# Kernel optimization log

Hardware: AMD Instinct MI355X
Metric: run time of the kernel (lower is better)

The kernel has to match this reference:

```python
import jax, jax.numpy as jnp
import numpy as np

B, S, H, DH = 8, 2048, 16, 64
D = H * DH  # 1024; also the input feature dim
BIG_NEG = 1e8


def setup_inputs() -> dict:
    key = jax.random.key(0)
    ks = jax.random.split(key, 7)
    glorot = lambda k, shp: jax.random.normal(k, shp, jnp.float32) * np.sqrt(2.0 / (shp[0] + shp[1]))
    return {
        "Q_seq": jax.random.normal(ks[0], (B, S, D), jnp.float32),
        "K_seq": jax.random.normal(ks[1], (B, S, D), jnp.float32),
        "Q_mask": jnp.ones((B, S), jnp.float32),
        "K_mask": jnp.ones((B, S), jnp.float32),
        "WQ": glorot(ks[2], (D, D)),
        "WK": glorot(ks[3], (D, D)),
        "Wq": glorot(ks[4], (D, H)),
        "Wk": glorot(ks[5], (D, H)),
        "WP": glorot(ks[6], (D, D)),
    }


def reference(Q_seq, B_K_seq=None, **_unused):
    raise NotImplementedError  # placeholder overwritten below


def reference(Q_seq, K_seq, Q_mask, K_mask, WQ, WK, Wq, Wk, WP):
    scale = 1.0 / (DH ** 0.5)
    b, s, _ = Q_seq.shape

    Q = Q_seq @ WQ                                        # (B,S,D)
    # query additive attention over the sequence, per head
    q_logits = jnp.einsum('bsd,dh->bhs', Q, Wq) * scale   # (B,H,S)
    q_logits = q_logits - (1.0 - Q_mask[:, None, :]) * BIG_NEG
    q_att = jax.nn.softmax(q_logits, axis=-1)

    Qh = Q.reshape(b, s, H, DH).transpose(0, 2, 1, 3)     # (B,H,S,DH)
    Kh = (K_seq @ WK).reshape(b, s, H, DH).transpose(0, 2, 1, 3)

    global_q = jnp.einsum('bhs,bhsd->bhd', q_att, Qh)     # (B,H,DH)
    QK = Kh * global_q[:, :, None, :]                     # (B,H,S,DH)

    # NOTE: original reshapes (B,H,S,DH) straight to (B,S,H*DH) WITHOUT a
    # transpose (head-mixing raw reshape) — replicated faithfully here.
    QK_flat = QK.reshape(b, s, H * DH)
    k_logits = jnp.einsum('bsd,dh->bhs', QK_flat, Wk) * scale
    k_logits = k_logits - (1.0 - K_mask[:, None, :]) * BIG_NEG
    k_att = jax.nn.softmax(k_logits, axis=-1)

    global_k = jnp.einsum('bhs,bhsd->bhd', k_att, QK)     # (B,H,DH)
    QKQ = global_k[:, :, None, :] * Qh                    # (B,H,S,DH)

    out = QKQ.transpose(0, 2, 1, 3).reshape(b, s, H * DH) @ WP
    out = out.reshape(b, s, H, DH).transpose(0, 2, 1, 3) + Qh   # (B,H,S,DH)
    out = out.transpose(0, 2, 1, 3).reshape(b, s, H * DH)       # (B,S,D)
    return out
```

## Files before the change

kernel.cpp:

```cpp
#include <hip/hip_runtime.h>
#include <cstdint>
#include <cstddef>


#define B_ 8
#define S_ 2048
#define H_ 16
#define D_ 1024
#define SCALE_ 0.125f
#define BIGNEG_ 1e8f

typedef __attribute__((ext_vector_type(8))) __bf16 bf16x8;
typedef __attribute__((ext_vector_type(4))) float f32x4;

__device__ __forceinline__ unsigned short f2bf(float f) {
  unsigned int u = __float_as_uint(f);
  u += 0x7FFFu + ((u >> 16) & 1u);
  return (unsigned short)(u >> 16);
}
__device__ __forceinline__ float bf2f(unsigned short h) {
  return __uint_as_float(((unsigned int)h) << 16);
}

__device__ __forceinline__ void gll16(const void* g, void* l) {
  __builtin_amdgcn_global_load_lds(
      (__attribute__((address_space(1))) void*)(uintptr_t)g,
      (__attribute__((address_space(3))) void*)(uintptr_t)l,
      16, 0, 0);
}

__global__ __launch_bounds__(256) void k_conv2(
    const float* __restrict__ in0, unsigned short* __restrict__ out0,
    const float* __restrict__ in1, unsigned short* __restrict__ out1, int n4) {
  int i = blockIdx.x * 256 + threadIdx.x;
  const float* in = in0;
  unsigned short* out = out0;
  if (i >= n4) { i -= n4; in = in1; out = out1; }
  float4 v = ((const float4*)in)[i];
  ushort4 o;
  o.x = f2bf(v.x); o.y = f2bf(v.y); o.z = f2bf(v.z); o.w = f2bf(v.w);
  ((ushort4*)out)[i] = o;
}

__global__ __launch_bounds__(256) void k_transpose3(
    const float* __restrict__ s0, unsigned short* __restrict__ d0,
    const float* __restrict__ s1, unsigned short* __restrict__ d1,
    const float* __restrict__ s2, unsigned short* __restrict__ d2,
    int K, int N) {
  const float* src = blockIdx.z == 0 ? s0 : (blockIdx.z == 1 ? s1 : s2);
  unsigned short* dst = blockIdx.z == 0 ? d0 : (blockIdx.z == 1 ? d1 : d2);
  __shared__ float tile[32][33];
  int n0 = blockIdx.x * 32, k0 = blockIdx.y * 32;
  int tx = threadIdx.x, ty = threadIdx.y;
#pragma unroll
  for (int i = 0; i < 4; i++) {
    int r = ty + i * 8;
    if (k0 + r < K && n0 + tx < N) tile[r][tx] = src[(size_t)(k0 + r) * N + n0 + tx];
  }
  __syncthreads();
#pragma unroll
  for (int i = 0; i < 4; i++) {
    int rn = ty + i * 8;
    if (n0 + rn < N && k0 + tx < K)
      dst[(size_t)(n0 + rn) * K + k0 + tx] = f2bf(tile[tx][rn]);
  }
}

__global__ __launch_bounds__(256) void k_transpose2(
    const float* __restrict__ s0, unsigned short* __restrict__ d0,
    const float* __restrict__ s1, unsigned short* __restrict__ d1,
    int K, int N) {
  const float* src = blockIdx.z == 0 ? s0 : s1;
  unsigned short* dst = blockIdx.z == 0 ? d0 : d1;
  __shared__ float tile[32][33];
  int n0 = blockIdx.x * 32, k0 = blockIdx.y * 32;
  int tx = threadIdx.x, ty = threadIdx.y;
#pragma unroll
  for (int i = 0; i < 4; i++) {
    int r = ty + i * 8;
    if (k0 + r < K && n0 + tx < N) tile[r][tx] = src[(size_t)(k0 + r) * N + n0 + tx];
  }
  __syncthreads();
#pragma unroll
  for (int i = 0; i < 4; i++) {
    int rn = ty + i * 8;
    if (n0 + rn < N && k0 + tx < K)
      dst[(size_t)(n0 + rn) * K + k0 + tx] = f2bf(tile[tx][rn]);
  }
}

__global__ __launch_bounds__(512, 2) void k_gemm256(
    const unsigned short* __restrict__ A, const unsigned short* __restrict__ Aalt,
    int asplit,
    const unsigned short* __restrict__ BTa, const unsigned short* __restrict__ BTb,
    int bstride, int bshift,
    unsigned short* __restrict__ Cbf, unsigned short* __restrict__ Calt,
    float* __restrict__ Cf, const unsigned short* __restrict__ Res,
    int N, int K, int ntiles) {
  __shared__ unsigned short lds[32768];
  int t = threadIdx.x;
  int lid = (blockIdx.x & 7) * ((int)gridDim.x >> 3) + (blockIdx.x >> 3);
  int mt = lid / ntiles, nt = lid - mt * ntiles;
  const unsigned short* BT = BTa;
  unsigned short* Cb = Cbf;
  if (mt >= asplit) { mt -= asplit; A = Aalt; BT = BTb; Cb = Calt; }
  if (bstride) BT += (size_t)(mt >> bshift) * (size_t)bstride;
  int m0 = mt * 256, n0 = nt * 256;
  int lane = t & 63, w = t >> 6;
  int wr = (w >> 2) * 128;
  int wc = (w & 3) * 64;
  int mq = lane & 15, q = lane >> 4;

  f32x4 zero = {0.f, 0.f, 0.f, 0.f};
  f32x4 acc[8][4];
#pragma unroll
  for (int i = 0; i < 8; i++)
#pragma unroll
    for (int j = 0; j < 4; j++) acc[i][j] = zero;

  const unsigned short* gA[2];
  const unsigned short* gB[2];
  int oA[2], oB[2];
#pragma unroll
  for (int p = 0; p < 2; p++) {
    int g = t + p * 512;
    int row2 = g >> 3, pre = (g & 7) ^ (row2 & 7);
    int r = row2 * 2 + (pre >> 2), oct = pre & 3;
    gA[p] = A + (size_t)(m0 + r) * K + oct * 8;
    gB[p] = BT + (size_t)(n0 + r) * K + oct * 8;
    oA[p] = g * 8;
    oB[p] = 8192 + g * 8;
  }

  int sA8 = ((((mq & 1) << 2) | q) ^ (mq >> 1)) * 8;
  int ra = (wr >> 1) + (mq >> 1);
  int rb = (wc >> 1) + (mq >> 1);

  int NT = K >> 5;
#pragma unroll
  for (int p = 0; p < 2; p++) gll16(gA[p], &lds[oA[p]]);
#pragma unroll
  for (int p = 0; p < 2; p++) gll16(gB[p], &lds[oB[p]]);
#pragma unroll
  for (int p = 0; p < 2; p++) gll16(gA[p] + 32, &lds[16384 + oA[p]]);
#pragma unroll
  for (int p = 0; p < 2; p++) gll16(gB[p] + 32, &lds[16384 + oB[p]]);

  for (int it = 0; it < NT; ++it) {
    int lbase = (it & 1) << 14;
    if (it < NT - 1) {
      asm volatile("s_waitcnt vmcnt(4)" ::: "memory");
    } else {
      asm volatile("s_waitcnt vmcnt(0)" ::: "memory");
    }
    __builtin_amdgcn_s_barrier();
    __builtin_amdgcn_sched_barrier(0);

    const unsigned short* la = &lds[lbase];
    const unsigned short* lb = &lds[lbase + 8192];
    bf16x8 av[8], bv[4];
#pragma unroll
    for (int i = 0; i < 4; i++)
      av[i] = *(const bf16x8*)&la[(ra + i * 8) * 64 + sA8];
#pragma unroll
    for (int j = 0; j < 4; j++)
      bv[j] = *(const bf16x8*)&lb[(rb + j * 8) * 64 + sA8];
    __builtin_amdgcn_sched_barrier(0);
#pragma unroll
    for (int i = 4; i < 8; i++)
      av[i] = *(const bf16x8*)&la[(ra + i * 8) * 64 + sA8];
    __builtin_amdgcn_sched_barrier(0);

    asm volatile("s_waitcnt lgkmcnt(4)" ::: "memory");
    __builtin_amdgcn_sched_barrier(0);
    __builtin_amdgcn_s_setprio(1);
#pragma unroll
    for (int i = 0; i < 4; i++)
#pragma unroll
      for (int j = 0; j < 4; j++)
        acc[i][j] = __builtin_amdgcn_mfma_f32_16x16x32_bf16(av[i], bv[j], acc[i][j], 0, 0, 0);
    __builtin_amdgcn_s_setprio(0);
    __builtin_amdgcn_sched_barrier(0);

    asm volatile("s_waitcnt lgkmcnt(0)" ::: "memory");
    __builtin_amdgcn_sched_barrier(0);
    __builtin_amdgcn_s_barrier();
    __builtin_amdgcn_sched_barrier(0);

    if (it + 2 < NT) {
      int k0 = (it + 2) * 32;
#pragma unroll
      for (int p = 0; p < 2; p++) gll16(gA[p] + k0, &lds[lbase + oA[p]]);
#pragma unroll
      for (int p = 0; p < 2; p++) gll16(gB[p] + k0, &lds[lbase + oB[p]]);
    }

    __builtin_amdgcn_s_setprio(1);
#pragma unroll
    for (int i = 4; i < 8; i++)
#pragma unroll
      for (int j = 0; j < 4; j++)
        acc[i][j] = __builtin_amdgcn_mfma_f32_16x16x32_bf16(av[i], bv[j], acc[i][j], 0, 0, 0);
    __builtin_amdgcn_s_setprio(0);
  }

#pragma unroll
  for (int i = 0; i < 8; i++)
#pragma unroll
    for (int j = 0; j < 4; j++)
#pragma unroll
      for (int r = 0; r < 4; r++) {
        int row = m0 + wr + i * 16 + q * 4 + r;
        int col = n0 + wc + j * 16 + mq;
        size_t o = (size_t)row * N + col;
        float v = acc[i][j][r];
        if (Res) v += bf2f(Res[o]);
        if (Cf) Cf[o] = v;
        if (Cb) Cb[o] = f2bf(v);
      }
}

__global__ __launch_bounds__(256) void k_logits16(
    const unsigned short* __restrict__ A,
    const unsigned short* __restrict__ BT16,
    const float* __restrict__ mask,
    float* __restrict__ outl,
    int K) {
  __shared__ unsigned short lA[64 * 32];
  int t = threadIdx.x;
  int m0 = blockIdx.x * 64;
  int lane = t & 63, w = t >> 6;
  int mq = lane & 15, q = lane >> 4;
  f32x4 acc = {0.f, 0.f, 0.f, 0.f};
  const unsigned short* gA = A + (size_t)(m0 + (t >> 2)) * K + (t & 3) * 8;
  unsigned short* pA = &lA[t * 8];
  for (int k0 = 0; k0 < K; k0 += 32) {
    gll16(gA + k0, pA);
    bf16x8 bv = *(const bf16x8*)&BT16[(size_t)mq * K + k0 + q * 8];
    __syncthreads();
    bf16x8 a0 = *(const bf16x8*)&lA[(w * 16 + mq) * 32 + q * 8];
    acc = __builtin_amdgcn_mfma_f32_16x16x32_bf16(a0, bv, acc, 0, 0, 0);
    __syncthreads();
  }
#pragma unroll
  for (int r = 0; r < 4; r++) {
    int row = m0 + w * 16 + q * 4 + r;
    int b = row >> 11, s = row & 2047;
    float v = acc[r] * SCALE_ - (1.0f - mask[row]) * BIGNEG_;
    outl[((size_t)(b * 16 + mq)) * 2048 + s] = v;
  }
}

__global__ __launch_bounds__(256) void k_logits16g(
    const unsigned short* __restrict__ Khbf,
    const unsigned short* __restrict__ WkT,
    const float* __restrict__ gq,
    const float* __restrict__ mask,
    float* __restrict__ outl) {
  __shared__ unsigned short lA[64 * 32];
  int t = threadIdx.x;
  int m0 = blockIdx.x * 64;
  int bb = m0 >> 11;
  int h2 = (m0 >> 7) & 15;
  int half = (m0 >> 6) & 1;
  int lane = t & 63, w = t >> 6;
  int mq = lane & 15, q = lane >> 4;
  f32x4 acc = {0.f, 0.f, 0.f, 0.f};
  int r0 = half * 64 + (t >> 2);
  int c0 = t & 3;
  const unsigned short* base = Khbf + (size_t)bb * 2048 * 1024 + h2 * 64;
  const float* gqb = gq + bb * 1024 + h2 * 64;
  unsigned short* pA = &lA[t * 8];
  for (int k0 = 0; k0 < 1024; k0 += 32) {
    int kc0 = k0 + c0 * 8;
    gll16(base + (size_t)(16 * r0 + (kc0 >> 6)) * 1024 + (kc0 & 63), pA);
    int kq = k0 + q * 8;
    bf16x8 wv = *(const bf16x8*)&WkT[(size_t)mq * 1024 + kq];
    float4 g0 = *(const float4*)&gqb[kq & 63];
    float4 g1 = *(const float4*)&gqb[(kq & 63) + 4];
    bf16x8 bv;
    bv[0] = (__bf16)((float)wv[0] * g0.x);
    bv[1] = (__bf16)((float)wv[1] * g0.y);
    bv[2] = (__bf16)((float)wv[2] * g0.z);
    bv[3] = (__bf16)((float)wv[3] * g0.w);
    bv[4] = (__bf16)((float)wv[4] * g1.x);
    bv[5] = (__bf16)((float)wv[5] * g1.y);
    bv[6] = (__bf16)((float)wv[6] * g1.z);
    bv[7] = (__bf16)((float)wv[7] * g1.w);
    __syncthreads();
    bf16x8 a0 = *(const bf16x8*)&lA[(w * 16 + mq) * 32 + q * 8];
    acc = __builtin_amdgcn_mfma_f32_16x16x32_bf16(a0, bv, acc, 0, 0, 0);
    __syncthreads();
  }
#pragma unroll
  for (int r = 0; r < 4; r++) {
    int row = m0 + w * 16 + q * 4 + r;
    int b = row >> 11, s = row & 2047;
    float v = acc[r] * SCALE_ - (1.0f - mask[row]) * BIGNEG_;
    outl[((size_t)(b * 16 + mq)) * 2048 + s] = v;
  }
}

__global__ __launch_bounds__(256) void k_softmax(float* __restrict__ logits) {
  __shared__ float red[8];
  int t = threadIdx.x;
  int lane = t & 63, w = t >> 6;
  float* lg = logits + (size_t)blockIdx.x * 2048;
  float4 a = ((const float4*)lg)[t];
  float4 b = ((const float4*)lg)[t + 256];
  float mx = fmaxf(fmaxf(fmaxf(a.x, a.y), fmaxf(a.z, a.w)),
                   fmaxf(fmaxf(b.x, b.y), fmaxf(b.z, b.w)));
#pragma unroll
  for (int off = 32; off > 0; off >>= 1) mx = fmaxf(mx, __shfl_down(mx, off, 64));
  if (lane == 0) red[w] = mx;
  __syncthreads();
  mx = fmaxf(fmaxf(red[0], red[1]), fmaxf(red[2], red[3]));
  float4 ea, eb;
  ea.x = expf(a.x - mx); ea.y = expf(a.y - mx); ea.z = expf(a.z - mx); ea.w = expf(a.w - mx);
  eb.x = expf(b.x - mx); eb.y = expf(b.y - mx); eb.z = expf(b.z - mx); eb.w = expf(b.w - mx);
  float ps = ea.x + ea.y + ea.z + ea.w + eb.x + eb.y + eb.z + eb.w;
#pragma unroll
  for (int off = 32; off > 0; off >>= 1) ps += __shfl_down(ps, off, 64);
  if (lane == 0) red[4 + w] = ps;
  __syncthreads();
  float inv = 1.0f / (red[4] + red[5] + red[6] + red[7]);
  ea.x *= inv; ea.y *= inv; ea.z *= inv; ea.w *= inv;
  eb.x *= inv; eb.y *= inv; eb.z *= inv; eb.w *= inv;
  ((float4*)lg)[t] = ea;
  ((float4*)lg)[t + 256] = eb;
}

__global__ __launch_bounds__(256) void k_poolpart(
    const float* __restrict__ att,
    const unsigned short* __restrict__ X,
    float* __restrict__ partial) {
  __shared__ float satt[32 * 16];
  int c = blockIdx.x, b = blockIdx.y;
  int t = threadIdx.x;
  for (int i = t; i < 512; i += 256) {
    int sl = i >> 4, h = i & 15;
    satt[i] = att[(((size_t)b * 16 + h) << 11) + c * 32 + sl];
  }
  __syncthreads();
  int h = t >> 4;
  const ushort4* xp = (const ushort4*)X + ((size_t)b * 2048 + c * 32) * 256 + t;
  float4 acc = {0.f, 0.f, 0.f, 0.f};
#pragma unroll 8
  for (int sl = 0; sl < 32; sl++) {
    float av = satt[sl * 16 + h];
    ushort4 xv = xp[sl * 256];
    acc.x += av * bf2f(xv.x);
    acc.y += av * bf2f(xv.y);
    acc.z += av * bf2f(xv.z);
    acc.w += av * bf2f(xv.w);
  }
  ((float4*)partial)[((size_t)b * 64 + c) * 256 + t] = acc;
}

__global__ __launch_bounds__(256) void k_poolfin(
    const float* __restrict__ partial,
    const float* __restrict__ gmul,
    float* __restrict__ outp) {
  int oi = blockIdx.x * 256 + threadIdx.x;
  int b = oi >> 10;
  const float* pp = partial + (size_t)b * 64 * 1024 + (oi & 1023);
  float s = 0.f;
#pragma unroll 8
  for (int c = 0; c < 64; c++) s += pp[(size_t)c * 1024];
  if (gmul) s *= gmul[oi];
  outp[oi] = s;
}

__global__ __launch_bounds__(256) void k_wpb(
    const unsigned short* __restrict__ WPT,
    const float* __restrict__ gk,
    unsigned short* __restrict__ WPb) {
  int i = blockIdx.x * 256 + threadIdx.x;
  int flat4 = i * 4;
  int b = flat4 >> 20;
  int rem = flat4 & 1048575;
  int k = rem & 1023;
  ushort4 wv = *(const ushort4*)&WPT[rem];
  float4 gv = *(const float4*)&gk[b * 1024 + k];
  ushort4 o;
  o.x = f2bf(bf2f(wv.x) * gv.x);
  o.y = f2bf(bf2f(wv.y) * gv.y);
  o.z = f2bf(bf2f(wv.z) * gv.z);
  o.w = f2bf(bf2f(wv.w) * gv.w);
  *(ushort4*)&WPb[flat4] = o;
}

extern "C" void kernel_launch(void* const* d_in, const int* in_sizes, int n_in,
                              void* d_out, int out_size, void* d_ws, size_t ws_size,
                              hipStream_t stream) {
  const float* Qseq  = (const float*)d_in[0];
  const float* Kseq  = (const float*)d_in[1];
  const float* Qmask = (const float*)d_in[2];
  const float* Kmask = (const float*)d_in[3];
  const float* WQ    = (const float*)d_in[4];
  const float* WK    = (const float*)d_in[5];
  const float* Wq    = (const float*)d_in[6];
  const float* Wk    = (const float*)d_in[7];
  const float* WP    = (const float*)d_in[8];
  float* out = (float*)d_out;

  const size_t SD = (size_t)B_ * S_ * D_;
  unsigned short* Qbf  = (unsigned short*)d_ws;
  unsigned short* Khbf = Qbf + SD;
  unsigned short* buf0 = Khbf + SD;
  unsigned short* WQT  = buf0 + SD;
  unsigned short* WKT  = WQT + (size_t)D_ * D_;
  unsigned short* WPT  = WKT + (size_t)D_ * D_;
  unsigned short* WqT  = WPT + (size_t)D_ * D_;
  unsigned short* WkT  = WqT + (size_t)H_ * D_;
  float* ql = (float*)(WkT + (size_t)H_ * D_);
  float* kl = ql + (size_t)B_ * H_ * S_;
  float* gq = kl + (size_t)B_ * H_ * S_;
  float* gk = gq + (size_t)B_ * D_;
  float* partial = (float*)buf0;
  unsigned short* WPb = buf0 + 2 * 1024 * 1024;
  unsigned short* Kstage = (unsigned short*)d_out;

  dim3 blk256(256);
  dim3 blk512(512);
  dim3 tblk(32, 8);
  int n4 = (int)(SD / 4);

  k_transpose3<<<dim3(32, 32, 3), tblk, 0, stream>>>(WQ, WQT, WK, WKT, WP, WPT, D_, D_);
  k_transpose2<<<dim3(1, 32, 2), tblk, 0, stream>>>(Wq, WqT, Wk, WkT, D_, H_);

  k_conv2<<<dim3(2 * ((n4 + 255) / 256)), blk256, 0, stream>>>(Qseq, buf0, Kseq, Kstage, n4);

  k_gemm256<<<dim3(512), blk512, 0, stream>>>(buf0, Kstage, 64, WQT, WKT, 0, 0,
                                              Qbf, Khbf, (float*)nullptr,
                                              (const unsigned short*)nullptr, D_, D_, 4);

  k_logits16<<<dim3(256), blk256, 0, stream>>>(Qbf, WqT, Qmask, ql, D_);
  k_softmax<<<dim3(128), blk256, 0, stream>>>(ql);
  k_poolpart<<<dim3(64, 8), blk256, 0, stream>>>(ql, Qbf, partial);
  k_poolfin<<<dim3(32), blk256, 0, stream>>>(partial, (const float*)nullptr, gq);

  k_logits16g<<<dim3(256), blk256, 0, stream>>>(Khbf, WkT, gq, Kmask, kl);
  k_softmax<<<dim3(128), blk256, 0, stream>>>(kl);
  k_poolpart<<<dim3(64, 8), blk256, 0, stream>>>(kl, Khbf, partial);
  k_poolfin<<<dim3(32), blk256, 0, stream>>>(partial, gq, gk);

  k_wpb<<<dim3(8192), blk256, 0, stream>>>(WPT, gk, WPb);
  k_gemm256<<<dim3(256), blk512, 0, stream>>>(Qbf, Qbf, 1 << 30, WPb, WPb, 1 << 20, 3,
                                              (unsigned short*)nullptr, (unsigned short*)nullptr,
                                              out, Qbf, D_, D_, 4);
}
```

Before: 387.6 us.

## Deepen GEMM LDS pipeline to four stages with split prefetch issue

Grows the 256x256 GEMM's LDS ring from two to four K-slices and prefetches three slices ahead. Global-to-LDS loads for each slice are split into two halves, each issued between the LDS fragment reads and the matching MFMA half. The goal is to hide more memory latency and cut the barrier stall at each iteration boundary. The cost is 128KB of LDS per block and launch bounds dropped to one block per CU, which lowers occupancy.

New measurement: 388.2 us. No clear change (+0.2%).

```diff
diff --git a/kernel.cpp b/kernel.cpp
--- a/kernel.cpp
+++ b/kernel.cpp
@@ -89,7 +89,7 @@
   }
 }
 
-__global__ __launch_bounds__(512, 2) void k_gemm256(
+__global__ __launch_bounds__(512, 1) void k_gemm256(
     const unsigned short* __restrict__ A, const unsigned short* __restrict__ Aalt,
     int asplit,
     const unsigned short* __restrict__ BTa, const unsigned short* __restrict__ BTb,
@@ -97,7 +97,7 @@
     unsigned short* __restrict__ Cbf, unsigned short* __restrict__ Calt,
     float* __restrict__ Cf, const unsigned short* __restrict__ Res,
     int N, int K, int ntiles) {
-  __shared__ unsigned short lds[32768];
+  __shared__ unsigned short lds[65536];
   int t = threadIdx.x;
   int lid = (blockIdx.x & 7) * ((int)gridDim.x >> 3) + (blockIdx.x >> 3);
   int mt = lid / ntiles, nt = lid - mt * ntiles;
@@ -138,70 +138,77 @@
 
   int NT = K >> 5;
 #pragma unroll
-  for (int p = 0; p < 2; p++) gll16(gA[p], &lds[oA[p]]);
-#pragma unroll
-  for (int p = 0; p < 2; p++) gll16(gB[p], &lds[oB[p]]);
-#pragma unroll
-  for (int p = 0; p < 2; p++) gll16(gA[p] + 32, &lds[16384 + oA[p]]);
-#pragma unroll
-  for (int p = 0; p < 2; p++) gll16(gB[p] + 32, &lds[16384 + oB[p]]);
-
-  for (int it = 0; it < NT; ++it) {
-    int lbase = (it & 1) << 14;
-    if (it < NT - 1) {
+  for (int Tt = 0; Tt < 3; Tt++) {
+    int ks = Tt * 32, sb = Tt << 14;
+#pragma unroll
+    for (int p = 0; p < 2; p++) gll16(gA[p] + ks, &lds[sb + oA[p]]);
+#pragma unroll
+    for (int p = 0; p < 2; p++) gll16(gB[p] + ks, &lds[sb + oB[p]]);
+  }
+  asm volatile("s_waitcnt vmcnt(8)" ::: "memory");
+  __builtin_amdgcn_s_barrier();
+  __builtin_amdgcn_sched_barrier(0);
+
+  for (int T = 0; T < NT; ++T) {
+    const int base = (T & 3) << 14;
+    const unsigned short* la = &lds[base];
+    const unsigned short* lb = &lds[base + 8192];
+    const int sbase = ((T + 3) & 3) << 14;
+    const int ks = (T + 3) * 32;
+    const bool stg = (T + 3 < NT);
+
+    bf16x8 avA[4], bv[4];
+#pragma unroll
+    for (int i = 0; i < 4; i++)
+      avA[i] = *(const bf16x8*)&la[(ra + i * 8) * 64 + sA8];
+#pragma unroll
+    for (int j = 0; j < 4; j++)
+      bv[j] = *(const bf16x8*)&lb[(rb + j * 8) * 64 + sA8];
+    if (stg) {
+      gll16(gA[0] + ks, &lds[sbase + oA[0]]);
+      gll16(gB[0] + ks, &lds[sbase + oB[0]]);
+    }
+    __builtin_amdgcn_s_barrier();
+    asm volatile("s_waitcnt lgkmcnt(0)" ::: "memory");
+    __builtin_amdgcn_sched_barrier(0);
+    __builtin_amdgcn_s_setprio(1);
+#pragma unroll
+    for (int i = 0; i < 4; i++)
+#pragma unroll
+      for (int j = 0; j < 4; j++)
+        acc[i][j] = __builtin_amdgcn_mfma_f32_16x16x32_bf16(avA[i], bv[j], acc[i][j], 0, 0, 0);
+    __builtin_amdgcn_s_setprio(0);
+    __builtin_amdgcn_sched_barrier(0);
+
+    bf16x8 avB[4];
+#pragma unroll
+    for (int i = 0; i < 4; i++)
+      avB[i] = *(const bf16x8*)&la[(ra + (i + 4) * 8) * 64 + sA8];
+    if (stg) {
+      gll16(gA[1] + ks, &lds[sbase + oA[1]]);
+      gll16(gB[1] + ks, &lds[sbase + oB[1]]);
+    }
+    __builtin_amdgcn_s_barrier();
+    asm volatile("s_waitcnt lgkmcnt(0)" ::: "memory");
+    __builtin_amdgcn_sched_barrier(0);
+    __builtin_amdgcn_s_setprio(1);
+#pragma unroll
+    for (int i = 0; i < 4; i++)
+#pragma unroll
+      for (int j = 0; j < 4; j++)
+        acc[i + 4][j] = __builtin_amdgcn_mfma_f32_16x16x32_bf16(avB[i], bv[j], acc[i + 4][j], 0, 0, 0);
+    __builtin_amdgcn_s_setprio(0);
+    __builtin_amdgcn_sched_barrier(0);
+
+    if (T <= NT - 4) {
+      asm volatile("s_waitcnt vmcnt(8)" ::: "memory");
+    } else if (T == NT - 3) {
       asm volatile("s_waitcnt vmcnt(4)" ::: "memory");
     } else {
       asm volatile("s_waitcnt vmcnt(0)" ::: "memory");
     }
     __builtin_amdgcn_s_barrier();
     __builtin_amdgcn_sched_barrier(0);
-
-    const unsigned short* la = &lds[lbase];
-    const unsigned short* lb = &lds[lbase + 8192];
-    bf16x8 av[8], bv[4];
-#pragma unroll
-    for (int i = 0; i < 4; i++)
-      av[i] = *(const bf16x8*)&la[(ra + i * 8) * 64 + sA8];
-#pragma unroll
-    for (int j = 0; j < 4; j++)
-      bv[j] = *(const bf16x8*)&lb[(rb + j * 8) * 64 + sA8];
-    __builtin_amdgcn_sched_barrier(0);
-#pragma unroll
-    for (int i = 4; i < 8; i++)
-      av[i] = *(const bf16x8*)&la[(ra + i * 8) * 64 + sA8];
-    __builtin_amdgcn_sched_barrier(0);
-
-    asm volatile("s_waitcnt lgkmcnt(4)" ::: "memory");
-    __builtin_amdgcn_sched_barrier(0);
-    __builtin_amdgcn_s_setprio(1);
-#pragma unroll
-    for (int i = 0; i < 4; i++)
-#pragma unroll
-      for (int j = 0; j < 4; j++)
-        acc[i][j] = __builtin_amdgcn_mfma_f32_16x16x32_bf16(av[i], bv[j], acc[i][j], 0, 0, 0);
-    __builtin_amdgcn_s_setprio(0);
-    __builtin_amdgcn_sched_barrier(0);
-
-    asm volatile("s_waitcnt lgkmcnt(0)" ::: "memory");
-    __builtin_amdgcn_sched_barrier(0);
-    __builtin_amdgcn_s_barrier();
-    __builtin_amdgcn_sched_barrier(0);
-
-    if (it + 2 < NT) {
-      int k0 = (it + 2) * 32;
-#pragma unroll
-      for (int p = 0; p < 2; p++) gll16(gA[p] + k0, &lds[lbase + oA[p]]);
-#pragma unroll
-      for (int p = 0; p < 2; p++) gll16(gB[p] + k0, &lds[lbase + oB[p]]);
-    }
-
-    __builtin_amdgcn_s_setprio(1);
-#pragma unroll
-    for (int i = 4; i < 8; i++)
-#pragma unroll
-      for (int j = 0; j < 4; j++)
-        acc[i][j] = __builtin_amdgcn_mfma_f32_16x16x32_bf16(av[i], bv[j], acc[i][j], 0, 0, 0);
-    __builtin_amdgcn_s_setprio(0);
   }
 
 #pragma unroll
```
